# Optimization experiments

Measured on AMD Instinct MI355X. Metric: run time of the kernel, lower is better.

The kernel has to match this reference:

```python
import jax, jax.numpy as jnp
import numpy as np

S, B, D, T = 256, 64, 1024, 64
BOS, EOS, PAD = 0, 1, 2


def setup_inputs() -> dict:
    key = jax.random.key(0)
    k1, k2, k3, k4, k5 = jax.random.split(key, 5)
    features = jax.random.normal(k1, (S, B, D), jnp.float32)
    tags = jax.random.randint(k2, (S, B), 0, T)
    # valid lengths in [2, S] so the recurrence and gold gather are well-defined
    seq_lens = jax.random.randint(k3, (B,), 2, S + 1)
    W = jax.random.normal(k4, (T, D), jnp.float32) * 0.02  # feat2tag weight
    b = jnp.zeros((T,), jnp.float32)                        # feat2tag bias
    transitions = jax.random.normal(k5, (T, T), jnp.float32) * 0.01
    return {"features": features, "tags": tags, "seq_lens": seq_lens,
            "W": W, "b": b, "transitions": transitions}


def reference(features, tags, seq_lens, W, b, transitions):
    s_len, b_size = features.shape[0], features.shape[1]
    n_tags = transitions.shape[0]
    # crf_scores[t, b, i, j] = emit[t, b, i] + transitions[i, j]
    emit = jnp.einsum('sbd,td->sbt', features, W) + b        # (S,B,T)
    crf = emit[:, :, :, None] + transitions[None, None]      # (S,B,T,T)

    # ---- gold path score ----
    pad_row = jnp.full((1, b_size), PAD, tags.dtype)
    nxt_tags = jnp.concatenate([tags[1:], pad_row], axis=0)  # (S,B)
    flat_ix = tags * n_tags + nxt_tags                       # (S,B)
    step_sc = jnp.take_along_axis(
        crf.reshape(s_len, b_size, n_tags * n_tags),
        flat_ix[:, :, None], axis=2)[..., 0]                 # (S,B)
    cum = jnp.cumsum(step_sc, axis=0)                        # (S,B)
    gold = cum[seq_lens - 1, jnp.arange(b_size)].sum()

    # ---- partition function via masked forward recurrence (scan over time) ----
    cur0 = crf[0, :, BOS, :]                                 # (B,T)
    active = jnp.arange(1, s_len)[:, None] < seq_lens[None, :]  # (S-1,B)

    def step(cur, xs):
        crf_t, act = xs                                      # (B,T,T), (B,)
        # logsumexp over previous tag i: cur[b,i] + crf_t[b,i,j]
        nxt = jax.nn.logsumexp(cur[:, :, None] + crf_t, axis=1)  # (B,T)
        return jnp.where(act[:, None], nxt, cur), None

    cur, _ = jax.lax.scan(step, cur0, (crf[1:], active))
    return cur[:, EOS].sum() - gold
```

## Files before the change

kernel.cpp:

```cpp
#include <hip/hip_runtime.h>

#define SLEN 256
#define NB   64
#define ND   1024
#define NT   64

typedef float f32x4  __attribute__((ext_vector_type(4)));
typedef short bf16x8 __attribute__((ext_vector_type(8)));
typedef __fp16 f16x8 __attribute__((ext_vector_type(8)));
typedef __fp16 f16x2 __attribute__((ext_vector_type(2)));
typedef unsigned int u32;
typedef u32 u32x2 __attribute__((ext_vector_type(2)));
typedef u32 u32x4 __attribute__((ext_vector_type(4)));
typedef int  i32x4 __attribute__((ext_vector_type(4)));

__device__ __forceinline__ u32 cvt_pk_bf16(float lo, float hi) {
  u32 r;
  asm("v_cvt_pk_bf16_f32 %0, %1, %2" : "=v"(r) : "v"(lo), "v"(hi));
  return r;
}

__device__ __forceinline__ u32 cvt_pk_f16(float lo, float hi) {
  union { f16x2 h; u32 u; } c;
  c.h = __builtin_amdgcn_cvt_pkrtz(lo, hi);
  return c.u;
}

__device__ __forceinline__ unsigned short f2bf(float f) {
  u32 u = __float_as_uint(f);
  return (unsigned short)((u + 0x7FFFu + ((u >> 16) & 1u)) >> 16);
}

__device__ __forceinline__ bf16x8 pack_bf16x8(f32x4 a, f32x4 b) {
  union { u32 u[4]; bf16x8 v; } r;
  r.u[0] = cvt_pk_bf16(a.x, a.y);
  r.u[1] = cvt_pk_bf16(a.z, a.w);
  r.u[2] = cvt_pk_bf16(b.x, b.y);
  r.u[3] = cvt_pk_bf16(b.z, b.w);
  return r.v;
}

__device__ __forceinline__ f32x4 vmax4(f32x4 a, f32x4 b) {
  f32x4 r;
  r.x = fmaxf(a.x, b.x); r.y = fmaxf(a.y, b.y);
  r.z = fmaxf(a.z, b.z); r.w = fmaxf(a.w, b.w);
  return r;
}

__global__ __launch_bounds__(256) void prep(const float* __restrict__ W,
                                            const float* __restrict__ trans,
                                            unsigned short* __restrict__ Wb3,
                                            u32* __restrict__ Ebuf,
                                            float* __restrict__ out) {
  if (blockIdx.x < 256) {
    int o  = blockIdx.x * 256 + threadIdx.x;
    int e  = o & 7;
    int l  = (o >> 3) & 63;
    int f  = (o >> 9) & 3;
    int k0 = o >> 11;
    int t  = f * 16 + (l & 15);
    int k  = k0 * 32 + ((l >> 4) << 3) + e;
    Wb3[o] = f2bf(W[t * ND + k]);
    return;
  }
  const int tid = threadIdx.x;
  if (tid == 0) out[0] = 0.f;
  const int l = tid & 63, wd = tid >> 6;
  const int q = l >> 4, c = l & 15;
#pragma unroll
  for (int mt = 0; mt < 4; ++mt)
#pragma unroll
    for (int kf = 0; kf < 2; ++kf) {
      float v0 = __expf(trans[(32 * kf + 8 * q + 2 * wd)     * NT + 16 * mt + c]) * 0.015625f;
      float v1 = __expf(trans[(32 * kf + 8 * q + 2 * wd + 1) * NT + 16 * mt + c]) * 0.015625f;
      Ebuf[(mt * 2 + kf) * 256 + l * 4 + wd] = cvt_pk_f16(v0, v1);
    }
}

__global__ __launch_bounds__(256) void emit_gemm(const float* __restrict__ F,
                                                 const unsigned short* __restrict__ Wb3,
                                                 const float* __restrict__ bias,
                                                 unsigned short* __restrict__ xbuf) {
  const int lane = threadIdx.x & 63;
  const int wv   = (blockIdx.x * 256 + threadIdx.x) >> 6;
  const int r0   = wv * 16;
  const int m    = lane & 15;
  const int kg   = lane >> 4;
  const float* arow = F + (size_t)(r0 + m) * ND + kg * 8;
  const bf16x8* bptr = reinterpret_cast<const bf16x8*>(Wb3) + lane;

  f32x4 acc0 = {0.f, 0.f, 0.f, 0.f};
  f32x4 acc1 = acc0, acc2 = acc0, acc3 = acc0;

  for (int g = 0; g < 32; g += 4) {
    f32x4  a[4][2];
    bf16x8 bb[4][4];
#pragma unroll
    for (int qq = 0; qq < 4; ++qq) {
      a[qq][0] = *(const f32x4*)(arow + (g + qq) * 32);
      a[qq][1] = *(const f32x4*)(arow + (g + qq) * 32 + 4);
#pragma unroll
      for (int f = 0; f < 4; ++f) bb[qq][f] = bptr[((g + qq) * 4 + f) * 64];
    }
#pragma unroll
    for (int qq = 0; qq < 4; ++qq) {
      bf16x8 af = pack_bf16x8(a[qq][0], a[qq][1]);
      acc0 = __builtin_amdgcn_mfma_f32_16x16x32_bf16(af, bb[qq][0], acc0, 0, 0, 0);
      acc1 = __builtin_amdgcn_mfma_f32_16x16x32_bf16(af, bb[qq][1], acc1, 0, 0, 0);
      acc2 = __builtin_amdgcn_mfma_f32_16x16x32_bf16(af, bb[qq][2], acc2, 0, 0, 0);
      acc3 = __builtin_amdgcn_mfma_f32_16x16x32_bf16(af, bb[qq][3], acc3, 0, 0, 0);
    }
  }

  const float bv0 = bias[m], bv1 = bias[16 + m], bv2 = bias[32 + m], bv3 = bias[48 + m];
  unsigned short* op = xbuf + (size_t)(r0 + kg * 4) * NT + m;
#pragma unroll
  for (int r = 0; r < 4; ++r) {
    op[r * NT +  0] = f2bf(__expf(acc0[r] + bv0));
    op[r * NT + 16] = f2bf(__expf(acc1[r] + bv1));
    op[r * NT + 32] = f2bf(__expf(acc2[r] + bv2));
    op[r * NT + 48] = f2bf(__expf(acc3[r] + bv3));
  }
}

__global__ __launch_bounds__(256, 2) void chunk_prod(
    const unsigned short* __restrict__ xbuf, const float* __restrict__ trans,
    const u32* __restrict__ Ebuf, const int* __restrict__ tags,
    const int* __restrict__ seq_lens, unsigned short* __restrict__ Gout,
    int* __restrict__ Gscale, float* __restrict__ Gpart) {
  __shared__ float trs[64 * 68];
  __shared__ unsigned short xlds[34 * 64];
  const int b   = blockIdx.x >> 3;
  const int k   = blockIdx.x & 7;
  const int tid = threadIdx.x;
  const int wid = tid >> 6;
  const int l   = tid & 63;
  const int q   = l >> 4, c = l & 15;

  const int L = seq_lens[b];

  {
    int tp  = tid >> 3;
    int cg  = (tid & 7) * 8;
    const u32x4* s4 = (const u32x4*)(xbuf + ((size_t)((32 * k + tp) * NB + b)) * NT + cg);
    *(u32x4*)(xlds + tp * 64 + cg) = *s4;
  }

  if (wid == 0) {
    float gp = 0.f;
    int s = 32 * k + (l & 31);
    if (l < 32 && s < L) {
      int tg = tags[s * NB + b];
      int nx = (s + 1 < SLEN) ? tags[(s + 1) * NB + b] : 2;
      float xv = __uint_as_float((u32)xbuf[(size_t)(s * NB + b) * NT + tg] << 16);
      gp = __logf(xv) + trans[tg * NT + nx];
    }
    gp += __shfl_xor(gp, 1, 64);
    gp += __shfl_xor(gp, 2, 64);
    gp += __shfl_xor(gp, 4, 64);
    gp += __shfl_xor(gp, 8, 64);
    gp += __shfl_xor(gp, 16, 64);
    if (l == 0) Gpart[b * 8 + k] = gp;
  }

  union uf { u32x4 u; f16x8 v; };
  uf ef[4][2];
#pragma unroll
  for (int mt = 0; mt < 4; ++mt)
#pragma unroll
    for (int kf = 0; kf < 2; ++kf)
      ef[mt][kf].u = *(const u32x4*)(Ebuf + (mt * 2 + kf) * 256 + l * 4);

  f32x4 g0 = {0,0,0,0}, g1 = g0, g2 = g0, g3 = g0;
  {
    int r = c - 4 * q;
    if (r >= 0 && r < 4) {
      float one = 1.0f;
      if (wid == 0) g0[r & 3] = one;
      else if (wid == 1) g1[r & 3] = one;
      else if (wid == 2) g2[r & 3] = one;
      else g3[r & 3] = one;
    }
  }

  int tbeg = 32 * k; if (tbeg < 1) tbeg = 1;
  int tend = 32 * k + 32; if (tend > L) tend = L;
  int exw = 0;

  __syncthreads();

#define SWAPQ(A, B) do {                                                  \
    asm("v_permlane32_swap_b32 %0, %1" : "+v"(A), "+v"(B));               \
    asm("v_permlane16_swap_b32 %0, %1" : "+v"(A), "+v"(B));               \
  } while (0)

#define LOADX(X, TP) do {                                                 \
    X[0] = *(const u32x2*)(xlds + (TP) * 64 + 4 * q);                     \
    X[1] = *(const u32x2*)(xlds + (TP) * 64 + 16 + 4 * q);                \
    X[2] = *(const u32x2*)(xlds + (TP) * 64 + 32 + 4 * q);                \
    X[3] = *(const u32x2*)(xlds + (TP) * 64 + 48 + 4 * q);                \
  } while (0)

#define MULPK(P0, P1, G, XW) do {                                         \
    f32x4 xv;                                                             \
    xv.x = __uint_as_float(XW.x << 16);                                   \
    xv.y = __uint_as_float(XW.x & 0xFFFF0000u);                           \
    xv.z = __uint_as_float(XW.y << 16);                                   \
    xv.w = __uint_as_float(XW.y & 0xFFFF0000u);                           \
    f32x4 ww = G * xv;                                                    \
    P0 = cvt_pk_f16(ww.x, ww.y);                                          \
    P1 = cvt_pk_f16(ww.z, ww.w);                                          \
  } while (0)

#define STEPF(X, T) do {                                                  \
    if ((((T) & 7) == 0) && ((T) != tbeg)) {         \
      f32x4 m4 = vmax4(vmax4(g0, g1), vmax4(g2, g3));                     \
      float mx = fmaxf(fmaxf(m4.x, m4.y), fmaxf(m4.z, m4.w));             \
      mx = fmaxf(mx, __shfl_xor(mx, 1, 64));                              \
      mx = fmaxf(mx, __shfl_xor(mx, 2, 64));                              \
      mx = fmaxf(mx, __shfl_xor(mx, 4, 64));                              \
      mx = fmaxf(mx, __shfl_xor(mx, 8, 64));                              \
      mx = fmaxf(mx, __shfl_xor(mx, 16, 64));                             \
      mx = fmaxf(mx, __shfl_xor(mx, 32, 64));                             \
      int ex = (int)((__float_as_uint(mx) >> 23) & 255u) - 127;           \
      float sc = __uint_as_float((u32)(127 - ex) << 23);                  \
      g0 *= sc; g1 *= sc; g2 *= sc; g3 *= sc; exw += ex;                  \
    }                                                                     \
    u32 p00, p01, p10, p11, p20, p21, p30, p31;                           \
    MULPK(p00, p01, g0, X[0]);                                            \
    MULPK(p10, p11, g1, X[1]);                                            \
    MULPK(p20, p21, g2, X[2]);                                            \
    MULPK(p30, p31, g3, X[3]);                                            \
    SWAPQ(p00, p10); SWAPQ(p01, p11); SWAPQ(p20, p30); SWAPQ(p21, p31);   \
    uf B0, B1;                                                            \
    B0.u[0] = p00; B0.u[1] = p01; B0.u[2] = p10; B0.u[3] = p11;           \
    B1.u[0] = p20; B1.u[1] = p21; B1.u[2] = p30; B1.u[3] = p31;           \
    const f32x4 zz = {0.f, 0.f, 0.f, 0.f};                                \
    g0 = __builtin_amdgcn_mfma_f32_16x16x32_f16(ef[0][0].v, B0.v, zz, 0, 0, 0); \
    g0 = __builtin_amdgcn_mfma_f32_16x16x32_f16(ef[0][1].v, B1.v, g0, 0, 0, 0); \
    g1 = __builtin_amdgcn_mfma_f32_16x16x32_f16(ef[1][0].v, B0.v, zz, 0, 0, 0); \
    g1 = __builtin_amdgcn_mfma_f32_16x16x32_f16(ef[1][1].v, B1.v, g1, 0, 0, 0); \
    g2 = __builtin_amdgcn_mfma_f32_16x16x32_f16(ef[2][0].v, B0.v, zz, 0, 0, 0); \
    g2 = __builtin_amdgcn_mfma_f32_16x16x32_f16(ef[2][1].v, B1.v, g2, 0, 0, 0); \
    g3 = __builtin_amdgcn_mfma_f32_16x16x32_f16(ef[3][0].v, B0.v, zz, 0, 0, 0); \
    g3 = __builtin_amdgcn_mfma_f32_16x16x32_f16(ef[3][1].v, B1.v, g3, 0, 0, 0); \
  } while (0)

  if (tbeg < tend) {
    u32x2 XA[4], XB[4];
    int tp  = tbeg - 32 * k;
    int tpe = tend - 32 * k;
    LOADX(XA, tp);
    for (; tp + 1 < tpe; tp += 2) {
      LOADX(XB, tp + 1);
      STEPF(XA, tp + 32 * k);
      LOADX(XA, tp + 2);
      STEPF(XB, tp + 1 + 32 * k);
    }
    if (tp < tpe) STEPF(XA, tp + 32 * k);
  }
#undef STEPF
#undef MULPK
#undef LOADX
#undef SWAPQ

  if (l == 0) Gscale[((size_t)b * 8 + k) * 4 + wid] = exw;

#pragma unroll
  for (int r = 0; r < 4; ++r) {
    trs[(4 * q + r) * 68      + 16 * wid + c] = g0[r];
    trs[(16 + 4 * q + r) * 68 + 16 * wid + c] = g1[r];
    trs[(32 + 4 * q + r) * 68 + 16 * wid + c] = g2[r];
    trs[(48 + 4 * q + r) * 68 + 16 * wid + c] = g3[r];
  }
  __syncthreads();
  {
    int row = tid >> 2, qt = tid & 3;
    const float* src = trs + row * 68 + qt * 16;
    u32 wp[8];
#pragma unroll
    for (int m = 0; m < 8; ++m) wp[m] = cvt_pk_bf16(src[2 * m], src[2 * m + 1]);
    u32x4* dst = (u32x4*)(Gout + (((size_t)(b * 8 + k) * 64 + row) * 64 + qt * 16));
    dst[0] = *(u32x4*)&wp[0];
    dst[1] = *(u32x4*)&wp[4];
  }
}

__global__ __launch_bounds__(64, 1) void chain_apply(
    const unsigned short* __restrict__ xbuf, const float* __restrict__ trans,
    const unsigned short* __restrict__ Gout, const int* __restrict__ Gscale,
    const float* __restrict__ Gpart, const int* __restrict__ seq_lens,
    float* __restrict__ out) {
  __shared__ __align__(16) float elds[64];
  const int b = blockIdx.x;
  const int j = threadIdx.x;
  const int L = seq_lens[b];

  float gp = (j < 8) ? Gpart[b * 8 + j] : 0.f;
  gp += __shfl_xor(gp, 1, 64);
  gp += __shfl_xor(gp, 2, 64);
  gp += __shfl_xor(gp, 4, 64);

  float A    = __expf(trans[j]);
  float logZ = __logf(__uint_as_float((u32)xbuf[(size_t)b * NT] << 16));

  const unsigned short* gbase = Gout + (size_t)b * 8 * 4096 + (size_t)j * 64;
  const i32x4* sbase = (const i32x4*)(Gscale + (size_t)b * 8 * 4);
  u32x4 gc[8], gn[8];
  i32x4 scc, scn;
#pragma unroll
  for (int m = 0; m < 8; ++m) gc[m] = *((const u32x4*)gbase + m);
  scc = sbase[0];

  const float C6 = 6.f * 0.6931471805599453f;

  for (int k = 0; k < 8; ++k) {
    if (k < 7) {
      const u32x4* gb2 = (const u32x4*)(gbase + (size_t)(k + 1) * 4096);
#pragma unroll
      for (int m = 0; m < 8; ++m) gn[m] = gb2[m];
      scn = sbase[k + 1];
    }
    int tb = 32 * k; if (tb < 1) tb = 1;
    int te = 32 * k + 32; if (te > L) te = L;
    int n = te - tb;
    if (n > 0) {
      elds[j] = A;
      float sA0 = 0.f, sA1 = 0.f, sA2 = 0.f, sA3 = 0.f;
      float sB0 = 0.f, sB1 = 0.f, sB2 = 0.f, sB3 = 0.f;
#pragma unroll
      for (int m = 0; m < 8; ++m) {
        f32x4 av0 = *(const f32x4*)(elds + 8 * m);
        f32x4 av1 = *(const f32x4*)(elds + 8 * m + 4);
        u32x4 w = gc[m];
        float a0, a1;
        a0 = fmaf(av0.x, __uint_as_float(w.x << 16),         0.f);
        a0 = fmaf(av0.y, __uint_as_float(w.x & 0xFFFF0000u), a0);
        a0 = fmaf(av0.z, __uint_as_float(w.y << 16),         a0);
        a0 = fmaf(av0.w, __uint_as_float(w.y & 0xFFFF0000u), a0);
        a1 = fmaf(av1.x, __uint_as_float(w.z << 16),         0.f);
        a1 = fmaf(av1.y, __uint_as_float(w.z & 0xFFFF0000u), a1);
        a1 = fmaf(av1.z, __uint_as_float(w.w << 16),         a1);
        a1 = fmaf(av1.w, __uint_as_float(w.w & 0xFFFF0000u), a1);
        switch (m >> 1) {
          case 0: if (m & 1) { sB0 += a0 + a1; } else { sA0 += a0 + a1; } break;
          case 1: if (m & 1) { sB1 += a0 + a1; } else { sA1 += a0 + a1; } break;
          case 2: if (m & 1) { sB2 += a0 + a1; } else { sA2 += a0 + a1; } break;
          default: if (m & 1) { sB3 += a0 + a1; } else { sA3 += a0 + a1; } break;
        }
      }
      float sc0 = __uint_as_float((u32)(127 + scc.x) << 23);
      float sc1 = __uint_as_float((u32)(127 + scc.y) << 23);
      float sc2 = __uint_as_float((u32)(127 + scc.z) << 23);
      float sc3 = __uint_as_float((u32)(127 + scc.w) << 23);
      A = ((sA0 + sB0) * sc0 + (sA1 + sB1) * sc1)
        + ((sA2 + sB2) * sc2 + (sA3 + sB3) * sc3);
      logZ += C6 * (float)n;
      u32 bb = __builtin_amdgcn_readfirstlane(__float_as_uint(A));
      int ex = (int)((bb >> 23) & 255u) - 127;
      A *= __uint_as_float((u32)(127 - ex) << 23);
      logZ += (float)ex * 0.6931471805599453f;
    }
    if (k < 7) {
#pragma unroll
      for (int m = 0; m < 8; ++m) gc[m] = gn[m];
      scc = scn;
    }
  }

  float res = logZ + __logf(A);
  res = __shfl(res, 1, 64);
  if (j == 0) atomicAdd(out, res - gp);
}

extern "C" void kernel_launch(void* const* d_in, const int* in_sizes, int n_in,
                              void* d_out, int out_size, void* d_ws, size_t ws_size,
                              hipStream_t stream) {
  const float* F     = (const float*)d_in[0];
  const int*   tags  = (const int*)  d_in[1];
  const int*   seq   = (const int*)  d_in[2];
  const float* W     = (const float*)d_in[3];
  const float* bias  = (const float*)d_in[4];
  const float* trans = (const float*)d_in[5];
  float* out = (float*)d_out;

  char* ws = (char*)d_ws;
  unsigned short* xbuf   = (unsigned short*)ws;
  unsigned short* Wb3    = (unsigned short*)(ws + 2228224);
  u32*            Ebuf   = (u32*)(ws + 2359296);
  unsigned short* Gout   = (unsigned short*)(ws + 2367488);
  int*            Gscale = (int*)(ws + 6561792);
  float*          Gpart  = (float*)(ws + 6569984);

  prep       <<<257, 256, 0, stream>>>(W, trans, Wb3, Ebuf, out);
  emit_gemm  <<<256, 256, 0, stream>>>(F, Wb3, bias, xbuf);
  chunk_prod <<<512, 256, 0, stream>>>(xbuf, trans, Ebuf, tags, seq, Gout, Gscale, Gpart);
  chain_apply<<<64,   64, 0, stream>>>(xbuf, trans, Gout, Gscale, Gpart, seq, out);
}
```

Before: 44.77 us.

## Split emit GEMM K dimension across wave pairs with LDS reduction

The emit GEMM now gives each 16-row strip to two waves, each covering half of the 1024-wide K dimension. The partial accumulators are combined through shared memory before the bias, exp and bf16 store, and the grid doubles to 512 blocks. The aim is more waves in flight, so more memory parallelism when streaming the large feature matrix. The cost is an LDS round trip, a block barrier, and half the waves idling during the epilogue. Separately, the transition-exp packing switches from round-toward-zero to round-to-nearest f16 conversion, a precision tweak.

Result: no change. 44.96 us (+0.4%).

```diff
diff --git a/kernel.cpp b/kernel.cpp
--- a/kernel.cpp
+++ b/kernel.cpp
@@ -23,6 +23,13 @@
 __device__ __forceinline__ u32 cvt_pk_f16(float lo, float hi) {
   union { f16x2 h; u32 u; } c;
   c.h = __builtin_amdgcn_cvt_pkrtz(lo, hi);
+  return c.u;
+}
+
+__device__ __forceinline__ u32 pack_f16_rne(float lo, float hi) {
+  union { _Float16 h[2]; u32 u; } c;
+  c.h[0] = (_Float16)lo;
+  c.h[1] = (_Float16)hi;
   return c.u;
 }
 
@@ -73,7 +80,7 @@
     for (int kf = 0; kf < 2; ++kf) {
       float v0 = __expf(trans[(32 * kf + 8 * q + 2 * wd)     * NT + 16 * mt + c]) * 0.015625f;
       float v1 = __expf(trans[(32 * kf + 8 * q + 2 * wd + 1) * NT + 16 * mt + c]) * 0.015625f;
-      Ebuf[(mt * 2 + kf) * 256 + l * 4 + wd] = cvt_pk_f16(v0, v1);
+      Ebuf[(mt * 2 + kf) * 256 + l * 4 + wd] = pack_f16_rne(v0, v1);
     }
 }
 
@@ -81,18 +88,22 @@
                                                  const unsigned short* __restrict__ Wb3,
                                                  const float* __restrict__ bias,
                                                  unsigned short* __restrict__ xbuf) {
-  const int lane = threadIdx.x & 63;
-  const int wv   = (blockIdx.x * 256 + threadIdx.x) >> 6;
-  const int r0   = wv * 16;
-  const int m    = lane & 15;
-  const int kg   = lane >> 4;
-  const float* arow = F + (size_t)(r0 + m) * ND + kg * 8;
-  const bf16x8* bptr = reinterpret_cast<const bf16x8*>(Wb3) + lane;
+  __shared__ float comb[4][64][17];
+  const int tid = threadIdx.x;
+  const int w   = tid >> 6;
+  const int l   = tid & 63;
+  const int q   = l >> 4;
+  const int c   = l & 15;
+  const int strip = blockIdx.x * 2 + (w >> 1);
+  const int kh    = w & 1;
+
+  const float* arow = F + (size_t)(strip * 16 + c) * ND + kh * 512 + q * 8;
+  const bf16x8* bptr = reinterpret_cast<const bf16x8*>(Wb3) + l;
 
   f32x4 acc0 = {0.f, 0.f, 0.f, 0.f};
   f32x4 acc1 = acc0, acc2 = acc0, acc3 = acc0;
 
-  for (int g = 0; g < 32; g += 4) {
+  for (int g = 0; g < 16; g += 4) {
     f32x4  a[4][2];
     bf16x8 bb[4][4];
 #pragma unroll
@@ -100,7 +111,8 @@
       a[qq][0] = *(const f32x4*)(arow + (g + qq) * 32);
       a[qq][1] = *(const f32x4*)(arow + (g + qq) * 32 + 4);
 #pragma unroll
-      for (int f = 0; f < 4; ++f) bb[qq][f] = bptr[((g + qq) * 4 + f) * 64];
+      for (int f = 0; f < 4; ++f)
+        bb[qq][f] = bptr[((kh * 16 + g + qq) * 4 + f) * 64];
     }
 #pragma unroll
     for (int qq = 0; qq < 4; ++qq) {
@@ -112,14 +124,31 @@
     }
   }
 
-  const float bv0 = bias[m], bv1 = bias[16 + m], bv2 = bias[32 + m], bv3 = bias[48 + m];
-  unsigned short* op = xbuf + (size_t)(r0 + kg * 4) * NT + m;
 #pragma unroll
   for (int r = 0; r < 4; ++r) {
-    op[r * NT +  0] = f2bf(__expf(acc0[r] + bv0));
-    op[r * NT + 16] = f2bf(__expf(acc1[r] + bv1));
-    op[r * NT + 32] = f2bf(__expf(acc2[r] + bv2));
-    op[r * NT + 48] = f2bf(__expf(acc3[r] + bv3));
+    comb[w][l][r]      = acc0[r];
+    comb[w][l][4 + r]  = acc1[r];
+    comb[w][l][8 + r]  = acc2[r];
+    comb[w][l][12 + r] = acc3[r];
+  }
+  __syncthreads();
+  if (kh == 0) {
+#pragma unroll
+    for (int r = 0; r < 4; ++r) {
+      acc0[r] += comb[w ^ 1][l][r];
+      acc1[r] += comb[w ^ 1][l][4 + r];
+      acc2[r] += comb[w ^ 1][l][8 + r];
+      acc3[r] += comb[w ^ 1][l][12 + r];
+    }
+    const float bv0 = bias[c], bv1 = bias[16 + c], bv2 = bias[32 + c], bv3 = bias[48 + c];
+    unsigned short* op = xbuf + (size_t)(strip * 16 + q * 4) * NT + c;
+#pragma unroll
+    for (int r = 0; r < 4; ++r) {
+      op[r * NT +  0] = f2bf(__expf(acc0[r] + bv0));
+      op[r * NT + 16] = f2bf(__expf(acc1[r] + bv1));
+      op[r * NT + 32] = f2bf(__expf(acc2[r] + bv2));
+      op[r * NT + 48] = f2bf(__expf(acc3[r] + bv3));
+    }
   }
 }
 
@@ -393,7 +422,7 @@
   float*          Gpart  = (float*)(ws + 6569984);
 
   prep       <<<257, 256, 0, stream>>>(W, trans, Wb3, Ebuf, out);
-  emit_gemm  <<<256, 256, 0, stream>>>(F, Wb3, bias, xbuf);
+  emit_gemm  <<<512, 256, 0, stream>>>(F, Wb3, bias, xbuf);
   chunk_prod <<<512, 256, 0, stream>>>(xbuf, trans, Ebuf, tags, seq, Gout, Gscale, Gpart);
   chain_apply<<<64,   64, 0, stream>>>(xbuf, trans, Gout, Gscale, Gpart, seq, out);
 }
```

## Split emit GEMM K across waves with LDS-staged bf16 features and reduction

Applied to the files above, without the earlier changes.

The emit GEMM used one wave per 16-row tile, and each wave looped over the full K=1024 reading strided fp32 rows. Now each block handles 16 rows. The block stages the rows into padded LDS as bf16 with coalesced loads, each of the four waves covers a quarter of K, and the partial accumulators are reduced through LDS before the bias+exp epilogue. This quadruples the grid to 1024 blocks for better latency hiding, at the cost of LDS traffic and extra barriers. The prep kernel also switches from round-toward-zero to round-to-nearest f16 packing for the transition exponentials.

After: 45.70 us. 1.02x slower.

```diff
diff --git a/kernel.cpp b/kernel.cpp
--- a/kernel.cpp
+++ b/kernel.cpp
@@ -4,6 +4,7 @@
 #define NB   64
 #define ND   1024
 #define NT   64
+#define APAD 1032
 
 typedef float f32x4  __attribute__((ext_vector_type(4)));
 typedef short bf16x8 __attribute__((ext_vector_type(8)));
@@ -26,18 +27,16 @@
   return c.u;
 }
 
+__device__ __forceinline__ u32 pack_f16_rne(float lo, float hi) {
+  union { _Float16 h[2]; u32 u; } c;
+  c.h[0] = (_Float16)lo;
+  c.h[1] = (_Float16)hi;
+  return c.u;
+}
+
 __device__ __forceinline__ unsigned short f2bf(float f) {
   u32 u = __float_as_uint(f);
   return (unsigned short)((u + 0x7FFFu + ((u >> 16) & 1u)) >> 16);
-}
-
-__device__ __forceinline__ bf16x8 pack_bf16x8(f32x4 a, f32x4 b) {
-  union { u32 u[4]; bf16x8 v; } r;
-  r.u[0] = cvt_pk_bf16(a.x, a.y);
-  r.u[1] = cvt_pk_bf16(a.z, a.w);
-  r.u[2] = cvt_pk_bf16(b.x, b.y);
-  r.u[3] = cvt_pk_bf16(b.z, b.w);
-  return r.v;
 }
 
 __device__ __forceinline__ f32x4 vmax4(f32x4 a, f32x4 b) {
@@ -73,7 +72,7 @@
     for (int kf = 0; kf < 2; ++kf) {
       float v0 = __expf(trans[(32 * kf + 8 * q + 2 * wd)     * NT + 16 * mt + c]) * 0.015625f;
       float v1 = __expf(trans[(32 * kf + 8 * q + 2 * wd + 1) * NT + 16 * mt + c]) * 0.015625f;
-      Ebuf[(mt * 2 + kf) * 256 + l * 4 + wd] = cvt_pk_f16(v0, v1);
+      Ebuf[(mt * 2 + kf) * 256 + l * 4 + wd] = pack_f16_rne(v0, v1);
     }
 }
 
@@ -81,45 +80,69 @@
                                                  const unsigned short* __restrict__ Wb3,
                                                  const float* __restrict__ bias,
                                                  unsigned short* __restrict__ xbuf) {
-  const int lane = threadIdx.x & 63;
-  const int wv   = (blockIdx.x * 256 + threadIdx.x) >> 6;
-  const int r0   = wv * 16;
-  const int m    = lane & 15;
-  const int kg   = lane >> 4;
-  const float* arow = F + (size_t)(r0 + m) * ND + kg * 8;
-  const bf16x8* bptr = reinterpret_cast<const bf16x8*>(Wb3) + lane;
+  __shared__ union ShU {
+    unsigned short a[16 * APAD];
+    float comb[4][64][17];
+  } sh;
+  const int tid = threadIdx.x;
+  const int w   = tid >> 6;
+  const int l   = tid & 63;
+  const int q   = l >> 4;
+  const int c   = l & 15;
+
+  const int blk = blockIdx.x;
+  const float* fb = F + (size_t)blk * 16 * ND;
+
+#pragma unroll 8
+  for (int i = 0; i < 16; ++i) {
+    f32x4 v = *(const f32x4*)(fb + i * ND + tid * 4);
+    u32x2 p;
+    p.x = cvt_pk_bf16(v.x, v.y);
+    p.y = cvt_pk_bf16(v.z, v.w);
+    *(u32x2*)(sh.a + i * APAD + tid * 4) = p;
+  }
+  __syncthreads();
 
   f32x4 acc0 = {0.f, 0.f, 0.f, 0.f};
   f32x4 acc1 = acc0, acc2 = acc0, acc3 = acc0;
-
-  for (int g = 0; g < 32; g += 4) {
-    f32x4  a[4][2];
-    bf16x8 bb[4][4];
-#pragma unroll
-    for (int qq = 0; qq < 4; ++qq) {
-      a[qq][0] = *(const f32x4*)(arow + (g + qq) * 32);
-      a[qq][1] = *(const f32x4*)(arow + (g + qq) * 32 + 4);
-#pragma unroll
-      for (int f = 0; f < 4; ++f) bb[qq][f] = bptr[((g + qq) * 4 + f) * 64];
-    }
-#pragma unroll
-    for (int qq = 0; qq < 4; ++qq) {
-      bf16x8 af = pack_bf16x8(a[qq][0], a[qq][1]);
-      acc0 = __builtin_amdgcn_mfma_f32_16x16x32_bf16(af, bb[qq][0], acc0, 0, 0, 0);
-      acc1 = __builtin_amdgcn_mfma_f32_16x16x32_bf16(af, bb[qq][1], acc1, 0, 0, 0);
-      acc2 = __builtin_amdgcn_mfma_f32_16x16x32_bf16(af, bb[qq][2], acc2, 0, 0, 0);
-      acc3 = __builtin_amdgcn_mfma_f32_16x16x32_bf16(af, bb[qq][3], acc3, 0, 0, 0);
-    }
-  }
-
-  const float bv0 = bias[m], bv1 = bias[16 + m], bv2 = bias[32 + m], bv3 = bias[48 + m];
-  unsigned short* op = xbuf + (size_t)(r0 + kg * 4) * NT + m;
+  const bf16x8* bptr = reinterpret_cast<const bf16x8*>(Wb3) + l;
+  const unsigned short* arow = sh.a + c * APAD + q * 8;
+
+#pragma unroll
+  for (int g = 0; g < 8; ++g) {
+    int ks = w * 8 + g;
+    bf16x8 af = *(const bf16x8*)(arow + ks * 32);
+    bf16x8 b0 = bptr[(ks * 4 + 0) * 64];
+    bf16x8 b1 = bptr[(ks * 4 + 1) * 64];
+    bf16x8 b2 = bptr[(ks * 4 + 2) * 64];
+    bf16x8 b3 = bptr[(ks * 4 + 3) * 64];
+    acc0 = __builtin_amdgcn_mfma_f32_16x16x32_bf16(af, b0, acc0, 0, 0, 0);
+    acc1 = __builtin_amdgcn_mfma_f32_16x16x32_bf16(af, b1, acc1, 0, 0, 0);
+    acc2 = __builtin_amdgcn_mfma_f32_16x16x32_bf16(af, b2, acc2, 0, 0, 0);
+    acc3 = __builtin_amdgcn_mfma_f32_16x16x32_bf16(af, b3, acc3, 0, 0, 0);
+  }
+
+  __syncthreads();
 #pragma unroll
   for (int r = 0; r < 4; ++r) {
-    op[r * NT +  0] = f2bf(__expf(acc0[r] + bv0));
-    op[r * NT + 16] = f2bf(__expf(acc1[r] + bv1));
-    op[r * NT + 32] = f2bf(__expf(acc2[r] + bv2));
-    op[r * NT + 48] = f2bf(__expf(acc3[r] + bv3));
+    sh.comb[w][l][r]      = acc0[r];
+    sh.comb[w][l][4 + r]  = acc1[r];
+    sh.comb[w][l][8 + r]  = acc2[r];
+    sh.comb[w][l][12 + r] = acc3[r];
+  }
+  __syncthreads();
+
+  {
+    float s[4];
+#pragma unroll
+    for (int r = 0; r < 4; ++r)
+      s[r] = sh.comb[0][l][4 * w + r] + sh.comb[1][l][4 * w + r]
+           + sh.comb[2][l][4 * w + r] + sh.comb[3][l][4 * w + r];
+    const float bv = bias[16 * w + c];
+    unsigned short* op = xbuf + (size_t)(blk * 16 + q * 4) * NT + 16 * w + c;
+#pragma unroll
+    for (int r = 0; r < 4; ++r)
+      op[r * NT] = f2bf(__expf(s[r] + bv));
   }
 }
 
@@ -392,8 +415,8 @@
   int*            Gscale = (int*)(ws + 6561792);
   float*          Gpart  = (float*)(ws + 6569984);
 
-  prep       <<<257, 256, 0, stream>>>(W, trans, Wb3, Ebuf, out);
-  emit_gemm  <<<256, 256, 0, stream>>>(F, Wb3, bias, xbuf);
-  chunk_prod <<<512, 256, 0, stream>>>(xbuf, trans, Ebuf, tags, seq, Gout, Gscale, Gpart);
-  chain_apply<<<64,   64, 0, stream>>>(xbuf, trans, Gout, Gscale, Gpart, seq, out);
-}
+  prep       <<<257,  256, 0, stream>>>(W, trans, Wb3, Ebuf, out);
+  emit_gemm  <<<1024, 256, 0, stream>>>(F, Wb3, bias, xbuf);
+  chunk_prod <<<512,  256, 0, stream>>>(xbuf, trans, Ebuf, tags, seq, Gout, Gscale, Gpart);
+  chain_apply<<<64,    64, 0, stream>>>(xbuf, trans, Gout, Gscale, Gpart, seq, out);
+}
```
